# Performance work log

Hardware: AMD Instinct MI355X
Metric: run time of the kernel (lower is better)

The kernel has to match this reference:

```python
import jax, jax.numpy as jnp
import numpy as np

EPS = 1e-3  # BatchNorm eps from module

def _bn(x, g, b, m, v):
    # torch BatchNorm1d (eval): (x - mean) / sqrt(var + eps) * weight + bias
    return (x - m) * (g / jnp.sqrt(v + EPS)) + b

def setup_inputs() -> dict:
    key = jax.random.key(0)
    ks = jax.random.split(key, 16)
    N, Cin, Cout, S = 1_000_000, 16, 64, 20_000
    inputs = jax.random.normal(ks[0], (N, Cin), dtype=jnp.float32)
    unq_inv = jax.random.randint(ks[1], (N,), 0, S, dtype=jnp.int32)

    def bn_params(k, c):
        k1, k2, k3, k4 = jax.random.split(k, 4)
        return (1.0 + 0.01 * jax.random.normal(k1, (c,), jnp.float32),
                0.01 * jax.random.normal(k2, (c,), jnp.float32),
                0.01 * jax.random.normal(k3, (c,), jnp.float32),
                jax.random.uniform(k4, (c,), jnp.float32, 0.5, 1.5))

    W1 = 0.1 * jax.random.normal(ks[2], (Cin, Cout), jnp.float32)
    g1, b1, m1, v1 = bn_params(ks[3], Cout)
    W2a = 0.1 * jax.random.normal(ks[4], (Cin, 2 * Cout), jnp.float32)
    g2a, b2a, m2a, v2a = bn_params(ks[5], 2 * Cout)
    W2b = 0.1 * jax.random.normal(ks[6], (2 * Cout, Cout), jnp.float32)
    g2b, b2b, m2b, v2b = bn_params(ks[7], Cout)

    return dict(inputs=inputs, unq_inv=unq_inv, num_segments=S,
                W1=W1, g1=g1, b1=b1, m1=m1, v1=v1,
                W2a=W2a, g2a=g2a, b2a=b2a, m2a=m2a, v2a=v2a,
                W2b=W2b, g2b=b2b * 0 + g2b, b2b=b2b, m2b=m2b, v2b=v2b)

def reference(inputs, unq_inv, num_segments,
              W1, g1, b1, m1, v1,
              W2a, g2a, b2a, m2a, v2a,
              W2b, g2b, b2b, m2b, v2b):
    # branch 1: Linear -> BN -> ReLU
    x = jax.nn.relu(_bn(inputs @ W1, g1, b1, m1, v1))            # [N, C]
    # branch 2: Linear -> BN -> ReLU -> Linear -> BN -> ReLU
    h = jax.nn.relu(_bn(inputs @ W2a, g2a, b2a, m2a, v2a))       # [N, 2C]
    x2 = jax.nn.relu(_bn(h @ W2b, g2b, b2b, m2b, v2b))           # [N, C]

    # segment reductions over group ids
    x_max = jax.ops.segment_max(x, unq_inv, num_segments=num_segments)  # [S, C]
    x_max = jnp.maximum(x_max, 0.0)  # empty segments -> 0 (x >= 0 post-ReLU)
    group_sum = jax.ops.segment_sum(x, unq_inv, num_segments=num_segments)  # [S, C]
    max_pool = jnp.max(x2, axis=0)                                # [C], global pool
    max_pool = jnp.broadcast_to(max_pool[None, :], x_max.shape)   # [S, C]

    feat = jnp.concatenate((group_sum, x_max, max_pool), axis=1)  # [S, 3C]
    # channel shuffle with groups=3
    S_, C3 = feat.shape
    feat = feat.reshape(S_, 3, C3 // 3).transpose(0, 2, 1).reshape(S_, C3)
    return feat
```

## Files before the change

kernel.cpp:

```cpp
#include <hip/hip_runtime.h>

#define EPS 1e-3f

#define OFF_T2B    7168
#define OFF_MPP    7232
#define OFF_MPF    11328
#define OFF_CNT    11392
#define OFF_OFFS   31408
#define OFF_CUR    51424
#define OFF_INPS   71424

typedef short short8 __attribute__((ext_vector_type(8)));
typedef float f32x4 __attribute__((ext_vector_type(4)));

union U4 { unsigned u[4]; short8 s8; uint4 u4; };

__device__ inline unsigned short f2bf(float f) {
    unsigned u = __float_as_uint(f);
    return (unsigned short)((u + 0x7FFFu + ((u >> 16) & 1u)) >> 16);
}

__global__ __launch_bounds__(256) void init_k(
    const float* __restrict__ W1,
    const float* __restrict__ g1, const float* __restrict__ b1,
    const float* __restrict__ m1, const float* __restrict__ v1,
    const float* __restrict__ W2a,
    const float* __restrict__ g2a, const float* __restrict__ b2a,
    const float* __restrict__ m2a, const float* __restrict__ v2a,
    const float* __restrict__ W2b,
    const float* __restrict__ g2b, const float* __restrict__ b2b,
    const float* __restrict__ m2b, const float* __restrict__ v2b,
    unsigned short* __restrict__ wsu, float* __restrict__ wsf,
    const int* __restrict__ unq, int* __restrict__ cnt, int N)
{
    const int t = threadIdx.x;
    if (blockIdx.x == 0) {
        for (int i = t; i < 2048; i += 256) {
            int mt = i >> 9, lane = (i >> 3) & 63, j = i & 7;
            int c = lane & 15, g = lane >> 4;
            int k = g * 8 + j, ch = mt * 16 + c;
            float s = g1[ch] * rsqrtf(v1[ch] + EPS);
            float val = (k < 16) ? W1[k * 64 + ch] * s
                      : (k == 16 ? b1[ch] - m1[ch] * s : 0.f);
            wsu[i] = f2bf(val);
        }
        for (int i = t; i < 4096; i += 256) {
            int mt = i >> 9, lane = (i >> 3) & 63, j = i & 7;
            int c = lane & 15, g = lane >> 4;
            int k = g * 8 + j, ch = mt * 16 + c;
            float s = g2a[ch] * rsqrtf(v2a[ch] + EPS);
            float val = (k < 16) ? W2a[k * 128 + ch] * s
                      : (k == 16 ? b2a[ch] - m2a[ch] * s : 0.f);
            wsu[2048 + i] = f2bf(val);
        }
        for (int i = t; i < 8192; i += 256) {
            int f = i >> 9, lane = (i >> 3) & 63, j = i & 7;
            int mt = f >> 2, ks = f & 3;
            int c = lane & 15, g = lane >> 4;
            int k = ks * 32 + g * 8 + j, ch = mt * 16 + c;
            float s = g2b[ch] * rsqrtf(v2b[ch] + EPS);
            wsu[6144 + i] = f2bf(W2b[k * 64 + ch] * s);
        }
        if (t < 64) {
            float s = g2b[t] * rsqrtf(v2b[t] + EPS);
            wsf[OFF_T2B + t] = b2b[t] - m2b[t] * s;
        }
    } else {
        const int i = (blockIdx.x - 1) * 256 + t;
        if (i < N) atomicAdd(&cnt[unq[i]], 1);
    }
}

__global__ __launch_bounds__(1024) void scan_k(
    const int* __restrict__ cnt, int* __restrict__ offs,
    int* __restrict__ cur, int S)
{
    __shared__ int tot[1024];
    const int t = threadIdx.x;
    const int E = (S + 1023) >> 10;
    const int i0 = t * E;
    int run = 0;
    for (int j = 0; j < E; ++j) {
        const int i = i0 + j;
        run += (i < S) ? cnt[i] : 0;
    }
    tot[t] = run;
    __syncthreads();
    for (int d = 1; d < 1024; d <<= 1) {
        int x = (t >= d) ? tot[t - d] : 0;
        __syncthreads();
        tot[t] += x;
        __syncthreads();
    }
    int base = (t == 0) ? 0 : tot[t - 1];
    for (int j = 0; j < E; ++j) {
        const int i = i0 + j;
        if (i < S) {
            offs[i] = base;
            cur[i]  = base;
            base += cnt[i];
        }
    }
    if (t == 1023) offs[S] = tot[1023];
}

__global__ __launch_bounds__(512, 2) void scatbr2_k(
    const float* __restrict__ inputs,
    const int*   __restrict__ unq,
    int*         __restrict__ cur,
    uint4*       __restrict__ inpS,
    const uint4* __restrict__ wsw,
    const float* __restrict__ wsf,
    float* __restrict__ mpp,
    int N)
{
    __shared__ __align__(16) char wlds[24576];
    __shared__ float t2bs[64];
    __shared__ float mpb[64];
    __shared__ __align__(16) char scrs[8][4096];

    const int tid = threadIdx.x;
    {
        #pragma unroll
        for (int u = 0; u < 3; ++u)
            reinterpret_cast<uint4*>(wlds)[u * 512 + tid] = wsw[256 + u * 512 + tid];
        if (tid < 64) { t2bs[tid] = wsf[OFF_T2B + tid]; mpb[tid] = 0.f; }
    }
    __syncthreads();

    const int wv   = tid >> 6;
    const int lane = tid & 63;
    const int c = lane & 15;
    const int g = lane >> 4;
    char* scr = scrs[wv];

    const long wave_pt0 = (long)blockIdx.x * 512 + (long)wv * 64;
    const long nrem_w = (long)N - wave_pt0;
    if (nrem_w <= 0) return;

    f32x4 t2br[4];
    #pragma unroll
    for (int mt = 0; mt < 4; ++mt)
        t2br[mt] = *reinterpret_cast<const f32x4*>(&t2bs[mt * 16 + g * 4]);

    const long ip = wave_pt0 + lane;
    const bool lane_ok = (ip < (long)N);
    int pos = 0;
    if (lane_ok) pos = atomicAdd(&cur[unq[ip]], 1);

    const f32x4 zero4 = {0.f, 0.f, 0.f, 0.f};
    float mp[16];
    #pragma unroll
    for (int j = 0; j < 16; ++j) mp[j] = 0.f;

    #pragma unroll
    for (int ti = 0; ti < 4; ++ti) {
        if ((long)ti * 16 >= nrem_w) break;
        const bool act = (long)(ti * 16 + c) < nrem_w;

        U4 bf;
        if (g < 2) {
            const long row = act ? (wave_pt0 + ti * 16 + c) : (long)(N - 1);
            const float4* p = reinterpret_cast<const float4*>(inputs + row * 16 + g * 8);
            float4 f0 = p[0], f1 = p[1];
            asm("v_cvt_pk_bf16_f32 %0, %1, %2" : "=v"(bf.u[0]) : "v"(f0.x), "v"(f0.y));
            asm("v_cvt_pk_bf16_f32 %0, %1, %2" : "=v"(bf.u[1]) : "v"(f0.z), "v"(f0.w));
            asm("v_cvt_pk_bf16_f32 %0, %1, %2" : "=v"(bf.u[2]) : "v"(f1.x), "v"(f1.y));
            asm("v_cvt_pk_bf16_f32 %0, %1, %2" : "=v"(bf.u[3]) : "v"(f1.z), "v"(f1.w));
            if (!act) { bf.u[0] = 0u; bf.u[1] = 0u; bf.u[2] = 0u; bf.u[3] = 0u; }
        } else {
            bf.u[0] = (g == 2 && act) ? 0x00003F80u : 0u;
            bf.u[1] = 0u; bf.u[2] = 0u; bf.u[3] = 0u;
        }

        const int posc = __shfl(pos, ti * 16 + c, 64);
        if (g < 2 && act)
            inpS[(size_t)posc * 2 + g] = bf.u4;

        #pragma unroll
        for (int mt = 0; mt < 8; ++mt) {
            short8 a = *reinterpret_cast<const short8*>(&wlds[(mt * 64 + lane) * 16]);
            f32x4 hT = __builtin_amdgcn_mfma_f32_16x16x32_bf16(a, bf.s8, zero4, 0, 0, 0);
            float h0 = fmaxf(hT[0], 0.f), h1 = fmaxf(hT[1], 0.f);
            float h2 = fmaxf(hT[2], 0.f), h3 = fmaxf(hT[3], 0.f);
            unsigned lo, hi;
            asm("v_cvt_pk_bf16_f32 %0, %1, %2" : "=v"(lo) : "v"(h0), "v"(h1));
            asm("v_cvt_pk_bf16_f32 %0, %1, %2" : "=v"(hi) : "v"(h2), "v"(h3));
            *reinterpret_cast<uint2*>(
                &scr[(unsigned)(c * 256 + mt * 32 + g * 8) ^ ((unsigned)(c & 7) << 4)])
                = make_uint2(lo, hi);
        }
        __builtin_amdgcn_wave_barrier();
        __builtin_amdgcn_sched_barrier(0);

        f32x4 y2t[4];
        #pragma unroll
        for (int mt = 0; mt < 4; ++mt) y2t[mt] = zero4;
        #pragma unroll
        for (int ks = 0; ks < 4; ++ks) {
            short8 hb = *reinterpret_cast<const short8*>(
                &scr[(unsigned)(c * 256 + ks * 64 + g * 16) ^ ((unsigned)(c & 7) << 4)]);
            #pragma unroll
            for (int mt = 0; mt < 4; ++mt) {
                short8 a = *reinterpret_cast<const short8*>(
                    &wlds[8192 + ((mt * 4 + ks) * 64 + lane) * 16]);
                y2t[mt] = __builtin_amdgcn_mfma_f32_16x16x32_bf16(a, hb, y2t[mt], 0, 0, 0);
            }
        }
        #pragma unroll
        for (int mt = 0; mt < 4; ++mt) {
            #pragma unroll
            for (int r = 0; r < 4; ++r) {
                float v = fmaxf(y2t[mt][r] + t2br[mt][r], 0.f);
                if (act) mp[mt * 4 + r] = fmaxf(mp[mt * 4 + r], v);
            }
        }
        __builtin_amdgcn_wave_barrier();
        __builtin_amdgcn_sched_barrier(0);
    }

    #pragma unroll
    for (int j = 0; j < 16; ++j) {
        float x = mp[j];
        x = fmaxf(x, __shfl_xor(x, 1, 64));
        x = fmaxf(x, __shfl_xor(x, 2, 64));
        x = fmaxf(x, __shfl_xor(x, 4, 64));
        x = fmaxf(x, __shfl_xor(x, 8, 64));
        mp[j] = x;
    }
    if (c == 0) {
        #pragma unroll
        for (int mt = 0; mt < 4; ++mt)
            #pragma unroll
            for (int r = 0; r < 4; ++r)
                atomicMax(reinterpret_cast<int*>(&mpb[mt * 16 + g * 4 + r]),
                          __float_as_int(mp[mt * 4 + r]));
    }
    __syncthreads();
    if (tid < 64)
        atomicMax(reinterpret_cast<int*>(mpp + (blockIdx.x & 63) * 64 + tid),
                  __float_as_int(mpb[tid]));
}

__global__ __launch_bounds__(64) void fin_k(
    const float* __restrict__ mpp, float* __restrict__ mpf)
{
    const int t = threadIdx.x;
    float m = 0.f;
    #pragma unroll
    for (int s = 0; s < 64; ++s)
        m = fmaxf(m, mpp[s * 64 + t]);
    mpf[t] = m;
}

__global__ __launch_bounds__(256, 6) void seg1_k(
    const uint4* __restrict__ inpS,
    const int*   __restrict__ offs,
    const uint4* __restrict__ wsw,
    const float* __restrict__ mpf,
    float* __restrict__ out,
    int S)
{
    __shared__ float scr3[4][192];

    const int tid  = threadIdx.x;
    const int wv   = tid >> 6;
    const int lane = tid & 63;
    const int seg  = blockIdx.x * 4 + wv;
    if (seg >= S) return;

    const int c = lane & 15;
    const int g = lane >> 4;

    short8 w1[4];
    #pragma unroll
    for (int mt = 0; mt < 4; ++mt) {
        U4 t; t.u4 = wsw[mt * 64 + lane]; w1[mt] = t.s8;
    }
    const float mpl = mpf[lane];

    const int su    = __builtin_amdgcn_readfirstlane(seg);
    const int start = offs[su];
    const int end   = offs[su + 1];

    const f32x4 zero4 = {0.f, 0.f, 0.f, 0.f};
    f32x4 as[4], am[4];
    #pragma unroll
    for (int mt = 0; mt < 4; ++mt) { as[mt] = zero4; am[mt] = zero4; }

    for (int base = start; base < end; base += 64) {
        const int nrem = end - base;
        #pragma unroll
        for (int ti = 0; ti < 4; ++ti) {
            if (ti * 16 >= nrem) break;
            const bool act = (ti * 16 + c) < nrem;

            U4 bf;
            if (g < 2) {
                const int row = min(base + ti * 16 + c, end - 1);
                uint4 q = inpS[(size_t)row * 2 + g];
                bf.u[0] = act ? q.x : 0u;
                bf.u[1] = act ? q.y : 0u;
                bf.u[2] = act ? q.z : 0u;
                bf.u[3] = act ? q.w : 0u;
            } else {
                bf.u[0] = (g == 2 && act) ? 0x00003F80u : 0u;
                bf.u[1] = 0u; bf.u[2] = 0u; bf.u[3] = 0u;
            }
            #pragma unroll
            for (int mt = 0; mt < 4; ++mt) {
                f32x4 y1t = __builtin_amdgcn_mfma_f32_16x16x32_bf16(w1[mt], bf.s8, zero4, 0, 0, 0);
                #pragma unroll
                for (int r = 0; r < 4; ++r) {
                    float v = fmaxf(y1t[r], 0.f);
                    as[mt][r] += v;
                    am[mt][r]  = fmaxf(am[mt][r], v);
                }
            }
        }
    }

    #pragma unroll
    for (int mt = 0; mt < 4; ++mt) {
        #pragma unroll
        for (int r = 0; r < 4; ++r) {
            float xs = as[mt][r], xm = am[mt][r];
            xs += __shfl_xor(xs, 1, 64);  xm = fmaxf(xm, __shfl_xor(xm, 1, 64));
            xs += __shfl_xor(xs, 2, 64);  xm = fmaxf(xm, __shfl_xor(xm, 2, 64));
            xs += __shfl_xor(xs, 4, 64);  xm = fmaxf(xm, __shfl_xor(xm, 4, 64));
            xs += __shfl_xor(xs, 8, 64);  xm = fmaxf(xm, __shfl_xor(xm, 8, 64));
            as[mt][r] = xs; am[mt][r] = xm;
        }
    }

    float* sr = scr3[wv];
    if (c == 0) {
        #pragma unroll
        for (int mt = 0; mt < 4; ++mt)
            #pragma unroll
            for (int r = 0; r < 4; ++r) {
                const int ch = mt * 16 + g * 4 + r;
                sr[ch * 3 + 0] = as[mt][r];
                sr[ch * 3 + 1] = am[mt][r];
            }
    }
    sr[lane * 3 + 2] = mpl;
    __builtin_amdgcn_wave_barrier();
    asm volatile("s_waitcnt lgkmcnt(0)" ::: "memory");
    __builtin_amdgcn_sched_barrier(0);

    float* o = out + (size_t)seg * 192;
    #pragma unroll
    for (int p = 0; p < 3; ++p)
        o[p * 64 + lane] = sr[p * 64 + lane];
}

extern "C" void kernel_launch(void* const* d_in, const int* in_sizes, int n_in,
                              void* d_out, int out_size, void* d_ws, size_t ws_size,
                              hipStream_t stream)
{
    const float* inputs = (const float*)d_in[0];
    const int*   unq    = (const int*)d_in[1];
    const float* W1  = (const float*)d_in[3];
    const float* g1  = (const float*)d_in[4];
    const float* b1  = (const float*)d_in[5];
    const float* m1  = (const float*)d_in[6];
    const float* v1  = (const float*)d_in[7];
    const float* W2a = (const float*)d_in[8];
    const float* g2a = (const float*)d_in[9];
    const float* b2a = (const float*)d_in[10];
    const float* m2a = (const float*)d_in[11];
    const float* v2a = (const float*)d_in[12];
    const float* W2b = (const float*)d_in[13];
    const float* g2b = (const float*)d_in[14];
    const float* b2b = (const float*)d_in[15];
    const float* m2b = (const float*)d_in[16];
    const float* v2b = (const float*)d_in[17];

    float* wsf = (float*)d_ws;
    float* out = (float*)d_out;
    const int N = in_sizes[0] / 16;
    const int S = out_size / 192;

    float* mpp  = wsf + OFF_MPP;
    float* mpf  = wsf + OFF_MPF;
    int*   cnt  = (int*)(wsf + OFF_CNT);
    int*   offs = (int*)(wsf + OFF_OFFS);
    int*   cur  = (int*)(wsf + OFF_CUR);
    uint4* inpS = (uint4*)(wsf + OFF_INPS);

    hipMemsetAsync(mpp, 0, (size_t)(OFF_CNT + 20016 - OFF_MPP) * sizeof(float), stream);

    init_k<<<1 + (N + 255) / 256, 256, 0, stream>>>(
        W1, g1, b1, m1, v1, W2a, g2a, b2a, m2a, v2a, W2b, g2b, b2b, m2b, v2b,
        (unsigned short*)d_ws, wsf, unq, cnt, N);

    scan_k<<<1, 1024, 0, stream>>>(cnt, offs, cur, S);

    scatbr2_k<<<(N + 511) / 512, 512, 0, stream>>>(inputs, unq, cur, inpS,
                                                   (const uint4*)d_ws, wsf, mpp, N);

    fin_k<<<1, 64, 0, stream>>>(mpp, mpf);

    seg1_k<<<(S + 3) / 4, 256, 0, stream>>>(inpS, offs, (const uint4*)d_ws,
                                            mpf, out, S);
}
```

Before: 218.7 us.

## Hold branch-2 weights in registers and double-buffer per-wave scratch in scatter kernel

Each wave now loads the W2a and W2b MFMA fragments straight into registers instead of staging them through shared memory. Blocks shrink from 512 to 256 threads with a different occupancy hint, and each wave gets a double-buffered, reorganized scratch layout. The final bias-plus-ReLU is moved out of the per-tile loop and applied once to the running max before the atomic reduction. This cuts LDS traffic and barriers, at the cost of higher register pressure and redundant global weight loads per wave.

Result: faster. 208.9 us (-4.5%).

```diff
diff --git a/kernel.cpp b/kernel.cpp
--- a/kernel.cpp
+++ b/kernel.cpp
@@ -104,7 +104,7 @@
     if (t == 1023) offs[S] = tot[1023];
 }
 
-__global__ __launch_bounds__(512, 2) void scatbr2_k(
+__global__ __launch_bounds__(256, 3) void scatbr2_k(
     const float* __restrict__ inputs,
     const int*   __restrict__ unq,
     int*         __restrict__ cur,
@@ -114,49 +114,46 @@
     float* __restrict__ mpp,
     int N)
 {
-    __shared__ __align__(16) char wlds[24576];
-    __shared__ float t2bs[64];
+    __shared__ __align__(16) char scrs[4][2][4096];
     __shared__ float mpb[64];
-    __shared__ __align__(16) char scrs[8][4096];
-
-    const int tid = threadIdx.x;
-    {
-        #pragma unroll
-        for (int u = 0; u < 3; ++u)
-            reinterpret_cast<uint4*>(wlds)[u * 512 + tid] = wsw[256 + u * 512 + tid];
-        if (tid < 64) { t2bs[tid] = wsf[OFF_T2B + tid]; mpb[tid] = 0.f; }
-    }
-    __syncthreads();
-
+
+    const int tid  = threadIdx.x;
     const int wv   = tid >> 6;
     const int lane = tid & 63;
     const int c = lane & 15;
     const int g = lane >> 4;
-    char* scr = scrs[wv];
-
-    const long wave_pt0 = (long)blockIdx.x * 512 + (long)wv * 64;
+
+    if (tid < 64) mpb[tid] = 0.f;
+    __syncthreads();
+
+    short8 w2a[8], w2b[16];
+    #pragma unroll
+    for (int mt = 0; mt < 8; ++mt) {
+        U4 t; t.u4 = wsw[256 + mt * 64 + lane]; w2a[mt] = t.s8;
+    }
+    #pragma unroll
+    for (int f = 0; f < 16; ++f) {
+        U4 t; t.u4 = wsw[768 + f * 64 + lane]; w2b[f] = t.s8;
+    }
+
+    const long wave_pt0 = (long)blockIdx.x * 256 + (long)wv * 64;
     const long nrem_w = (long)N - wave_pt0;
-    if (nrem_w <= 0) return;
-
-    f32x4 t2br[4];
-    #pragma unroll
-    for (int mt = 0; mt < 4; ++mt)
-        t2br[mt] = *reinterpret_cast<const f32x4*>(&t2bs[mt * 16 + g * 4]);
 
     const long ip = wave_pt0 + lane;
-    const bool lane_ok = (ip < (long)N);
+    const bool lane_ok = (ip < (long)N) && (nrem_w > 0);
     int pos = 0;
     if (lane_ok) pos = atomicAdd(&cur[unq[ip]], 1);
 
     const f32x4 zero4 = {0.f, 0.f, 0.f, 0.f};
     float mp[16];
     #pragma unroll
-    for (int j = 0; j < 16; ++j) mp[j] = 0.f;
+    for (int j = 0; j < 16; ++j) mp[j] = -3.0e38f;
 
     #pragma unroll
     for (int ti = 0; ti < 4; ++ti) {
         if ((long)ti * 16 >= nrem_w) break;
         const bool act = (long)(ti * 16 + c) < nrem_w;
+        char* scr = scrs[wv][ti & 1];
 
         U4 bf;
         if (g < 2) {
@@ -177,46 +174,39 @@
         if (g < 2 && act)
             inpS[(size_t)posc * 2 + g] = bf.u4;
 
+        __builtin_amdgcn_wave_barrier();
         #pragma unroll
         for (int mt = 0; mt < 8; ++mt) {
-            short8 a = *reinterpret_cast<const short8*>(&wlds[(mt * 64 + lane) * 16]);
-            f32x4 hT = __builtin_amdgcn_mfma_f32_16x16x32_bf16(a, bf.s8, zero4, 0, 0, 0);
+            f32x4 hT = __builtin_amdgcn_mfma_f32_16x16x32_bf16(w2a[mt], bf.s8, zero4, 0, 0, 0);
             float h0 = fmaxf(hT[0], 0.f), h1 = fmaxf(hT[1], 0.f);
             float h2 = fmaxf(hT[2], 0.f), h3 = fmaxf(hT[3], 0.f);
             unsigned lo, hi;
             asm("v_cvt_pk_bf16_f32 %0, %1, %2" : "=v"(lo) : "v"(h0), "v"(h1));
             asm("v_cvt_pk_bf16_f32 %0, %1, %2" : "=v"(hi) : "v"(h2), "v"(h3));
+            const int gw = 2 * (mt & 1) + (g >> 1);
             *reinterpret_cast<uint2*>(
-                &scr[(unsigned)(c * 256 + mt * 32 + g * 8) ^ ((unsigned)(c & 7) << 4)])
+                &scr[(mt >> 1) * 1024 + (gw * 16 + c) * 16 + (g & 1) * 8])
                 = make_uint2(lo, hi);
         }
         __builtin_amdgcn_wave_barrier();
-        __builtin_amdgcn_sched_barrier(0);
 
         f32x4 y2t[4];
         #pragma unroll
         for (int mt = 0; mt < 4; ++mt) y2t[mt] = zero4;
         #pragma unroll
         for (int ks = 0; ks < 4; ++ks) {
-            short8 hb = *reinterpret_cast<const short8*>(
-                &scr[(unsigned)(c * 256 + ks * 64 + g * 16) ^ ((unsigned)(c & 7) << 4)]);
-            #pragma unroll
-            for (int mt = 0; mt < 4; ++mt) {
-                short8 a = *reinterpret_cast<const short8*>(
-                    &wlds[8192 + ((mt * 4 + ks) * 64 + lane) * 16]);
-                y2t[mt] = __builtin_amdgcn_mfma_f32_16x16x32_bf16(a, hb, y2t[mt], 0, 0, 0);
-            }
+            short8 hb = *reinterpret_cast<const short8*>(&scr[ks * 1024 + lane * 16]);
+            #pragma unroll
+            for (int mt = 0; mt < 4; ++mt)
+                y2t[mt] = __builtin_amdgcn_mfma_f32_16x16x32_bf16(w2b[mt * 4 + ks], hb, y2t[mt], 0, 0, 0);
         }
         #pragma unroll
         for (int mt = 0; mt < 4; ++mt) {
             #pragma unroll
-            for (int r = 0; r < 4; ++r) {
-                float v = fmaxf(y2t[mt][r] + t2br[mt][r], 0.f);
-                if (act) mp[mt * 4 + r] = fmaxf(mp[mt * 4 + r], v);
-            }
+            for (int r = 0; r < 4; ++r)
+                mp[mt * 4 + r] = act ? fmaxf(mp[mt * 4 + r], y2t[mt][r]) : mp[mt * 4 + r];
         }
         __builtin_amdgcn_wave_barrier();
-        __builtin_amdgcn_sched_barrier(0);
     }
 
     #pragma unroll
@@ -232,9 +222,11 @@
         #pragma unroll
         for (int mt = 0; mt < 4; ++mt)
             #pragma unroll
-            for (int r = 0; r < 4; ++r)
-                atomicMax(reinterpret_cast<int*>(&mpb[mt * 16 + g * 4 + r]),
-                          __float_as_int(mp[mt * 4 + r]));
+            for (int r = 0; r < 4; ++r) {
+                const int ch = mt * 16 + g * 4 + r;
+                const float v = fmaxf(mp[mt * 4 + r] + wsf[OFF_T2B + ch], 0.f);
+                atomicMax(reinterpret_cast<int*>(&mpb[ch]), __float_as_int(v));
+            }
     }
     __syncthreads();
     if (tid < 64)
@@ -397,7 +389,7 @@
 
     scan_k<<<1, 1024, 0, stream>>>(cnt, offs, cur, S);
 
-    scatbr2_k<<<(N + 511) / 512, 512, 0, stream>>>(inputs, unq, cur, inpS,
+    scatbr2_k<<<(N + 255) / 256, 256, 0, stream>>>(inputs, unq, cur, inpS,
                                                    (const uint4*)d_ws, wsf, mpp, N);
 
     fin_k<<<1, 64, 0, stream>>>(mpp, mpf);
```
